# Optimization experiments

Hardware: AMD Instinct MI355X
Metric: run time of the kernel (lower is better)

## Reference

```python
import jax, jax.numpy as jnp
import numpy as np

H = 11          # hidden size
L = 5           # num layers
G = 4 * H       # gates (i,f,g,o) per PyTorch order


def run_dir(x, Wih, Whh, b, reverse):
    """Single-direction LSTM over x [B,T,D] -> [B,T,H]."""
    pre = jnp.einsum('btd,gd->btg', x, Wih) + b      # [B,T,4H] input projections
    pre = pre.transpose(1, 0, 2)                     # [T,B,4H]
    if reverse:
        pre = pre[::-1]
    B = x.shape[0]
    h0 = jnp.zeros((B, H), x.dtype)
    c0 = jnp.zeros((B, H), x.dtype)

    def step(carry, gt):
        h, c = carry
        g = gt + h @ Whh.T                           # [B,4H]
        i, f, gg, o = jnp.split(g, 4, axis=-1)
        i = jax.nn.sigmoid(i)
        f = jax.nn.sigmoid(f)
        gg = jnp.tanh(gg)
        o = jax.nn.sigmoid(o)
        c = f * c + i * gg
        h = o * jnp.tanh(c)
        return (h, c), h

    _, hs = jax.lax.scan(step, (h0, c0), pre)        # hs [T,B,H]
    if reverse:
        hs = hs[::-1]
    return hs.transpose(1, 0, 2)                     # [B,T,H]


def setup_inputs() -> dict:
    key = jax.random.key(0)
    ks = jax.random.split(key, 6)
    x = jax.random.normal(ks[0], (2048, 1, 32, 512), dtype=jnp.float32)
    # PyTorch LSTM params: layer0 input=1; layers1-4 input=2H (bidir concat)
    W_ih0 = jax.random.normal(ks[1], (2, G, 1), dtype=jnp.float32) * 0.2
    W_ih_rest = jax.random.normal(ks[2], (L - 1, 2, G, 2 * H), dtype=jnp.float32) * 0.1
    W_hh = jax.random.normal(ks[3], (L, 2, G, H), dtype=jnp.float32) * 0.1
    b_ih = jax.random.normal(ks[4], (L, 2, G), dtype=jnp.float32) * 0.05
    b_hh = jax.random.normal(ks[5], (L, 2, G), dtype=jnp.float32) * 0.05
    return {"x": x, "W_ih0": W_ih0, "W_ih_rest": W_ih_rest, "W_hh": W_hh,
            "b_ih": b_ih, "b_hh": b_hh}


def reference(x, W_ih0, W_ih_rest, W_hh, b_ih, b_hh):
    # x: [B, C=1, height, width] -> sum over height -> [B, C, W] -> [B, W, C]
    inp = x.sum(2).transpose(0, 2, 1)                # [B, W, 1]
    for l in range(L):
        outs = []
        for d in range(2):                           # 0=fwd, 1=bwd
            Wih = W_ih0[d] if l == 0 else W_ih_rest[l - 1, d]
            b = b_ih[l, d] + b_hh[l, d]
            outs.append(run_dir(inp, Wih, W_hh[l, d], b, reverse=(d == 1)))
        inp = jnp.concatenate(outs, axis=-1)         # [B, W, 2H]
    return inp
```

## Files before the change

### kernel.cpp

```cpp
#include <hip/hip_runtime.h>

constexpr int TT = 512;
constexpr int BB = 2048;
constexpr int HH = 11;
constexpr int GG = 44;
constexpr int NL = 5;

typedef float v2f __attribute__((ext_vector_type(2)));

__device__ __forceinline__ float dpp_q0(float v) {
    return __int_as_float(__builtin_amdgcn_mov_dpp(__float_as_int(v), 0x00, 0xF, 0xF, false));
}
__device__ __forceinline__ float dpp_q1(float v) {
    return __int_as_float(__builtin_amdgcn_mov_dpp(__float_as_int(v), 0x55, 0xF, 0xF, false));
}
__device__ __forceinline__ float dpp_q3(float v) {
    return __int_as_float(__builtin_amdgcn_mov_dpp(__float_as_int(v), 0xFF, 0xF, 0xF, false));
}
__device__ __forceinline__ float dpp_qswap2(float v) {
    return __int_as_float(__builtin_amdgcn_mov_dpp(__float_as_int(v), 0x4E, 0xF, 0xF, false));
}

__global__ void reduce_x(const float* __restrict__ x, float* __restrict__ inp) {
    int t = blockIdx.x * 256 + threadIdx.x;
    int b = blockIdx.y;
    const float* p = x + (size_t)b * 32 * TT + t;
    float s = 0.f;
#pragma unroll
    for (int k = 0; k < 32; k++) s += p[k * TT];
    inp[(size_t)b * TT + t] = s;
}

template <int IND>
__global__ __launch_bounds__(256, 4)
void lstm_layer(
    const float* __restrict__ xin,
    float* __restrict__ out,
    const float* __restrict__ Wih,
    const float* __restrict__ Whh,
    const float* __restrict__ bih,
    const float* __restrict__ bhh)
{
    constexpr int NP   = (IND > 1) ? IND / 2 : 1;
    constexpr int CH   = (IND == 1) ? 64 : 32;
    constexpr int NCH  = TT / CH;
    constexpr int NLD  = (CH * IND) / 64;
    constexpr int PERW = 64 + 2 * CH * IND;

    __shared__ float smem[4 * PERW];

    const float L2E   = 1.4426950408889634f;
    const float NL2E  = -L2E;
    const float N2L2E = -2.f * L2E;

    int tid  = threadIdx.x;
    int lane = tid & 63;
    int wid  = tid >> 6;
    int u = lane >> 2;
    int q = lane & 3;
    bool active = (u < HH);
    int grow = q * HH + u;

    int seq = __builtin_amdgcn_readfirstlane((int)blockIdx.x * 4 + wid);
    int b = seq >> 1;
    int d = seq & 1;

    float esc    = (q == 2) ? N2L2E : NL2E;
    float ascale = (q == 2) ? 2.f * N2L2E : 1.f;
    float aoff   = (q == 2) ? -N2L2E : 0.f;

    v2f   wih2[NP];
    float wih0 = 0.f;
    v2f   whh2[6];
    v2f   bias2;
    if (active) {
        const float* wi = Wih + (size_t)(d * GG + grow) * IND;
        if constexpr (IND == 1) {
            wih0 = wi[0] * esc;
        } else {
#pragma unroll
            for (int p = 0; p < NP; p++) wih2[p] = ((const v2f*)wi)[p] * esc;
        }
        const float* wh = Whh + (size_t)(d * GG + grow) * HH;
#pragma unroll
        for (int k = 0; k < 5; k++)
            whh2[k] = (v2f){wh[2 * k] * esc, wh[2 * k + 1] * esc};
        whh2[5] = (v2f){wh[10] * esc, 0.f};
        float bv = (bih[d * GG + grow] + bhh[d * GG + grow]) * esc;
        bias2 = (v2f){bv, 0.f};
    } else {
        if constexpr (IND != 1) {
#pragma unroll
            for (int p = 0; p < NP; p++) wih2[p] = (v2f){0.f, 0.f};
        }
#pragma unroll
        for (int k = 0; k < 6; k++) whh2[k] = (v2f){0.f, 0.f};
        bias2 = (v2f){0.f, 0.f};
    }

    v2f hp[6];
#pragma unroll
    for (int k = 0; k < 6; k++) hp[k] = (v2f){0.f, 0.f};
    float c = 0.f;

    const int ostep = d ? -22 : 22;
    float* op = out + (size_t)b * TT * 22 + (size_t)(d ? (TT - 1) * 22 : 0)
                    + d * HH + u;
    const bool doStore = (q == 0) && active;

    float* shh = smem + wid * PERW;
    float* xls = shh + 64;

    const float* gbase = xin + (size_t)b * TT * IND
                             + (size_t)(d ? (TT - CH) * IND : 0);
    const int gstep = d ? -(CH * IND) : (CH * IND);
    const int lstep = d ? -IND : IND;

    {
        float p0[NLD];
#pragma unroll
        for (int k = 0; k < NLD; k++) p0[k] = gbase[k * 64 + lane];
#pragma unroll
        for (int k = 0; k < NLD; k++) xls[k * 64 + lane] = p0[k];
    }
    int buf = 0;
    float* swc = xls;
    const float* lrow = swc + (d ? (CH - 1) * IND : 0);

    v2f   xA[NP], xB[NP];
    float xAs = 0.f, xBs = 0.f;
    if constexpr (IND == 1) {
        xAs = lrow[0];
    } else {
#pragma unroll
        for (int p = 0; p < NP; p++) xA[p] = ((const v2f*)lrow)[p];
    }

    const float* gnext = gbase + gstep;

#define LSTM_STEP(XC, XN, DOPF)                                               \
    do {                                                                      \
        v2f accA, accB;                                                       \
        float pre;                                                            \
        if constexpr (IND == 1) {                                             \
            accA = __builtin_elementwise_fma(hp[0], whh2[0], bias2);          \
            accB = hp[1] * whh2[1];                                           \
            _Pragma("unroll")                                                 \
            for (int k = 2; k < 6; k++) {                                     \
                if (k & 1) accB = __builtin_elementwise_fma(hp[k], whh2[k], accB);\
                else       accA = __builtin_elementwise_fma(hp[k], whh2[k], accA);\
            }                                                                 \
            v2f s = accA + accB;                                              \
            pre = fmaf(XC##s, wih0, s.x + s.y);                               \
            if (DOPF) { lrow += lstep; XN##s = lrow[0]; }                     \
        } else {                                                              \
               \
            accA = __builtin_elementwise_fma(XC[0], wih2[0], bias2);          \
            accB = XC[1] * wih2[1];                                           \
            _Pragma("unroll")                                                 \
            for (int p = 2; p < NP; p++) {                                    \
                if (p & 1) accB = __builtin_elementwise_fma(XC[p], wih2[p], accB);\
                else       accA = __builtin_elementwise_fma(XC[p], wih2[p], accA);\
            }                                                                 \
            if (DOPF) {              \
                lrow += lstep;                                                \
                _Pragma("unroll")                                             \
                for (int p = 0; p < NP; p++) XN[p] = ((const v2f*)lrow)[p];   \
            }                                                                 \
                                                              \
            _Pragma("unroll")                                                 \
            for (int k = 0; k < 6; k++) {                                     \
                if (k & 1) accB = __builtin_elementwise_fma(hp[k], whh2[k], accB);\
                else       accA = __builtin_elementwise_fma(hp[k], whh2[k], accA);\
            }                                                                 \
            v2f s = accA + accB;                                              \
            pre = s.x + s.y;                                                  \
        }                                                                     \
        float e   = __builtin_amdgcn_exp2f(pre);                              \
        float act = fmaf(ascale, __builtin_amdgcn_rcpf(1.f + e), aoff);       \
        float ig  = act * dpp_qswap2(act);                 \
        float igb = dpp_q0(ig);                                               \
        float fv  = dpp_q1(act);                                              \
        float ov  = dpp_q3(act);                                              \
        c = fmaf(fv, c, igb);                                                 \
        float e2 = __builtin_amdgcn_exp2f(c);                                 \
        float th = fmaf(2.f, __builtin_amdgcn_rcpf(1.f + e2), -1.f);          \
        float h  = ov * th;                                 \
        if (doStore) *op = h;                                                 \
        op += ostep;                                                          \
            \
        shh[lane] = h;                                                        \
        _Pragma("unroll")                                                     \
        for (int k = 0; k < 6; k++)                                           \
            hp[k] = (v2f){shh[8 * k], shh[8 * k + 4]};                        \
    } while (0)

    for (int ch = 0; ch < NCH; ch++) {
        const bool last = (ch + 1 == NCH);
        float pf[NLD];
        if (!last) {
#pragma unroll
            for (int k = 0; k < NLD; k++) pf[k] = gnext[k * 64 + lane];
        }
        for (int sl = 0; sl < CH - 2; sl += 2) {
            LSTM_STEP(xA, xB, true);
            LSTM_STEP(xB, xA, true);
        }
        LSTM_STEP(xA, xB, true);
        LSTM_STEP(xB, xA, false);
        if (!last) {
            float* swn = xls + ((buf ^ 1) ? CH * IND : 0);
#pragma unroll
            for (int k = 0; k < NLD; k++) swn[k * 64 + lane] = pf[k];
            buf ^= 1;
            swc = swn;
            lrow = swc + (d ? (CH - 1) * IND : 0);
            if constexpr (IND == 1) {
                xAs = lrow[0];
            } else {
#pragma unroll
                for (int p = 0; p < NP; p++) xA[p] = ((const v2f*)lrow)[p];
            }
            gnext += gstep;
        }
    }
#undef LSTM_STEP
}

extern "C" void kernel_launch(void* const* d_in, const int* in_sizes, int n_in,
                              void* d_out, int out_size, void* d_ws, size_t ws_size,
                              hipStream_t stream) {
    const float* x        = (const float*)d_in[0];
    const float* W_ih0    = (const float*)d_in[1];
    const float* W_ih_rest= (const float*)d_in[2];
    const float* W_hh     = (const float*)d_in[3];
    const float* b_ih     = (const float*)d_in[4];
    const float* b_hh     = (const float*)d_in[5];
    float* out = (float*)d_out;

    const size_t perB = (size_t)TT * 22 * sizeof(float);
    int chunk = BB;
    while (chunk > 2 && (size_t)chunk * perB > ws_size) chunk >>= 1;
    float* wsbuf = (float*)d_ws;

    for (int c0 = 0; c0 < BB; c0 += chunk) {
        const float* xc   = x + (size_t)c0 * 32 * TT;
        float*       outc = out + (size_t)c0 * TT * 22;
        const int nblk = (chunk * 2) / 4;

        reduce_x<<<dim3(2, chunk), 256, 0, stream>>>(xc, wsbuf);

        lstm_layer<1><<<nblk, 256, 0, stream>>>(wsbuf, outc, W_ih0, W_hh, b_ih, b_hh);

        for (int l = 1; l < NL; l++) {
            const float* src = (l & 1) ? outc : wsbuf;
            float*       dst = (l & 1) ? wsbuf : outc;
            lstm_layer<22><<<nblk, 256, 0, stream>>>(
                src, dst,
                W_ih_rest + (size_t)(l - 1) * 2 * GG * 22,
                W_hh + (size_t)l * 2 * GG * HH,
                b_ih + (size_t)l * 2 * GG,
                b_hh + (size_t)l * 2 * GG);
        }
    }
}
```

Baseline: 1.427 ms.

## Broadcast hidden state via readlane to SGPRs instead of LDS round trip

Replaces the per-step LDS write/read of the hidden state with inline-asm v_readlane into scalar registers feeding packed FMAs, removing an LDS store/load and its wait from the serial recurrence. It also re-lays the staged input rows into a padded, direction-normalized layout (row stride 24, reversed for backward) so each timestep's input row loads as 16-byte vectors with a constant positive stride. The cost is that readlane-to-SGPR-to-VALU dependencies can stall, and hardcoded SGPR clobbers s20-s31 constrain register allocation.

```diff
diff --git a/kernel.cpp b/kernel.cpp
--- a/kernel.cpp
+++ b/kernel.cpp
@@ -7,6 +7,7 @@
 constexpr int NL = 5;
 
 typedef float v2f __attribute__((ext_vector_type(2)));
+typedef float v4f __attribute__((ext_vector_type(4)));
 
 __device__ __forceinline__ float dpp_q0(float v) {
     return __int_as_float(__builtin_amdgcn_mov_dpp(__float_as_int(v), 0x00, 0xF, 0xF, false));
@@ -41,13 +42,14 @@
     const float* __restrict__ bih,
     const float* __restrict__ bhh)
 {
-    constexpr int NP   = (IND > 1) ? IND / 2 : 1;
-    constexpr int CH   = (IND == 1) ? 64 : 32;
-    constexpr int NCH  = TT / CH;
-    constexpr int NLD  = (CH * IND) / 64;
-    constexpr int PERW = 64 + 2 * CH * IND;
-
-    __shared__ float smem[4 * PERW];
+    constexpr int NP    = (IND > 1) ? IND / 2 : 1;
+    constexpr int CH    = (IND == 1) ? 64 : 32;
+    constexpr int NCH   = TT / CH;
+    constexpr int NLD   = (CH * IND) / 64;
+    constexpr int RS    = (IND == 1) ? 1 : 24;
+    constexpr int BUFSZ = CH * RS;
+
+    __shared__ __align__(16) float smem[4 * 2 * BUFSZ];
 
     const float L2E   = 1.4426950408889634f;
     const float NL2E  = -L2E;
@@ -98,9 +100,7 @@
         bias2 = (v2f){0.f, 0.f};
     }
 
-    v2f hp[6];
-#pragma unroll
-    for (int k = 0; k < 6; k++) hp[k] = (v2f){0.f, 0.f};
+    float hprev = 0.f;
     float c = 0.f;
 
     const int ostep = d ? -22 : 22;
@@ -108,53 +108,60 @@
                     + d * HH + u;
     const bool doStore = (q == 0) && active;
 
-    float* shh = smem + wid * PERW;
-    float* xls = shh + 64;
+    float* xls = smem + wid * (2 * BUFSZ);
 
     const float* gbase = xin + (size_t)b * TT * IND
                              + (size_t)(d ? (TT - CH) * IND : 0);
     const int gstep = d ? -(CH * IND) : (CH * IND);
-    const int lstep = d ? -IND : IND;
+
+    int wdw[NLD];
+#pragma unroll
+    for (int k = 0; k < NLD; k++) {
+        int p = k * 64 + lane;
+        int row = p / IND;
+        int col = p - row * IND;
+        int r2 = d ? (CH - 1 - row) : row;
+        wdw[k] = r2 * RS + col;
+    }
 
     {
         float p0[NLD];
 #pragma unroll
         for (int k = 0; k < NLD; k++) p0[k] = gbase[k * 64 + lane];
 #pragma unroll
-        for (int k = 0; k < NLD; k++) xls[k * 64 + lane] = p0[k];
+        for (int k = 0; k < NLD; k++) xls[wdw[k]] = p0[k];
     }
     int buf = 0;
-    float* swc = xls;
-    const float* lrow = swc + (d ? (CH - 1) * IND : 0);
+    const float* lrow = xls;
+    const float* gnext = gbase + gstep;
 
     v2f   xA[NP], xB[NP];
     float xAs = 0.f, xBs = 0.f;
-    if constexpr (IND == 1) {
-        xAs = lrow[0];
-    } else {
-#pragma unroll
-        for (int p = 0; p < NP; p++) xA[p] = ((const v2f*)lrow)[p];
-    }
-
-    const float* gnext = gbase + gstep;
+
+#define LOAD_ROW(DST, PTR)                                                    \
+    do {                                                                      \
+        if constexpr (IND == 1) {                                             \
+            DST##s = (PTR)[0];                                                \
+        } else {                                                              \
+            _Pragma("unroll")                                                 \
+            for (int i4 = 0; i4 < 5; i4++) {                                  \
+                v4f t4 = ((const v4f*)(PTR))[i4];                             \
+                DST[2 * i4]     = (v2f){t4.x, t4.y};                          \
+                DST[2 * i4 + 1] = (v2f){t4.z, t4.w};                          \
+            }                                                                 \
+            DST[10] = ((const v2f*)(PTR))[10];                                \
+        }                                                                     \
+    } while (0)
+
+    LOAD_ROW(xA, lrow);
 
 #define LSTM_STEP(XC, XN, DOPF)                                               \
     do {                                                                      \
         v2f accA, accB;                                                       \
-        float pre;                                                            \
         if constexpr (IND == 1) {                                             \
-            accA = __builtin_elementwise_fma(hp[0], whh2[0], bias2);          \
-            accB = hp[1] * whh2[1];                                           \
-            _Pragma("unroll")                                                 \
-            for (int k = 2; k < 6; k++) {                                     \
-                if (k & 1) accB = __builtin_elementwise_fma(hp[k], whh2[k], accB);\
-                else       accA = __builtin_elementwise_fma(hp[k], whh2[k], accA);\
-            }                                                                 \
-            v2f s = accA + accB;                                              \
-            pre = fmaf(XC##s, wih0, s.x + s.y);                               \
-            if (DOPF) { lrow += lstep; XN##s = lrow[0]; }                     \
+            accA = bias2;                                                     \
+            accB = (v2f){0.f, 0.f};                                           \
         } else {                                                              \
-               \
             accA = __builtin_elementwise_fma(XC[0], wih2[0], bias2);          \
             accB = XC[1] * wih2[1];                                           \
             _Pragma("unroll")                                                 \
@@ -162,23 +169,39 @@
                 if (p & 1) accB = __builtin_elementwise_fma(XC[p], wih2[p], accB);\
                 else       accA = __builtin_elementwise_fma(XC[p], wih2[p], accA);\
             }                                                                 \
-            if (DOPF) {              \
-                lrow += lstep;                                                \
-                _Pragma("unroll")                                             \
-                for (int p = 0; p < NP; p++) XN[p] = ((const v2f*)lrow)[p];   \
-            }                                                                 \
-                                                              \
-            _Pragma("unroll")                                                 \
-            for (int k = 0; k < 6; k++) {                                     \
-                if (k & 1) accB = __builtin_elementwise_fma(hp[k], whh2[k], accB);\
-                else       accA = __builtin_elementwise_fma(hp[k], whh2[k], accA);\
-            }                                                                 \
-            v2f s = accA + accB;                                              \
-            pre = s.x + s.y;                                                  \
         }                                                                     \
+        if (DOPF) { lrow += RS; LOAD_ROW(XN, lrow); }                         \
+            \
+        asm volatile(                                                         \
+            "v_readlane_b32 s20, %2, 0\n\t"                                   \
+            "v_readlane_b32 s21, %2, 4\n\t"                                   \
+            "v_readlane_b32 s22, %2, 8\n\t"                                   \
+            "v_readlane_b32 s23, %2, 12\n\t"                                  \
+            "v_readlane_b32 s24, %2, 16\n\t"                                  \
+            "v_readlane_b32 s25, %2, 20\n\t"                                  \
+            "v_readlane_b32 s26, %2, 24\n\t"                                  \
+            "v_readlane_b32 s27, %2, 28\n\t"                                  \
+            "v_readlane_b32 s28, %2, 32\n\t"                                  \
+            "v_readlane_b32 s29, %2, 36\n\t"                                  \
+            "v_readlane_b32 s30, %2, 40\n\t"                                  \
+            "v_readlane_b32 s31, %2, 44\n\t"                                  \
+            "v_pk_fma_f32 %0, s[20:21], %3, %0\n\t"                           \
+            "v_pk_fma_f32 %1, s[22:23], %4, %1\n\t"                           \
+            "v_pk_fma_f32 %0, s[24:25], %5, %0\n\t"                           \
+            "v_pk_fma_f32 %1, s[26:27], %6, %1\n\t"                           \
+            "v_pk_fma_f32 %0, s[28:29], %7, %0\n\t"                           \
+            "v_pk_fma_f32 %1, s[30:31], %8, %1"                               \
+            : "+v"(accA), "+v"(accB)                                          \
+            : "v"(hprev), "v"(whh2[0]), "v"(whh2[1]), "v"(whh2[2]),           \
+              "v"(whh2[3]), "v"(whh2[4]), "v"(whh2[5])                        \
+            : "s20","s21","s22","s23","s24","s25","s26","s27",                \
+              "s28","s29","s30","s31");                                       \
+        v2f s2 = accA + accB;                                                 \
+        float pre = s2.x + s2.y;                                              \
+        if constexpr (IND == 1) pre = fmaf(XC##s, wih0, pre);                 \
         float e   = __builtin_amdgcn_exp2f(pre);                              \
         float act = fmaf(ascale, __builtin_amdgcn_rcpf(1.f + e), aoff);       \
-        float ig  = act * dpp_qswap2(act);                 \
+        float ig  = act * dpp_qswap2(act);                  \
         float igb = dpp_q0(ig);                                               \
         float fv  = dpp_q1(act);                                              \
         float ov  = dpp_q3(act);                                              \
@@ -188,11 +211,7 @@
         float h  = ov * th;                                 \
         if (doStore) *op = h;                                                 \
         op += ostep;                                                          \
-            \
-        shh[lane] = h;                                                        \
-        _Pragma("unroll")                                                     \
-        for (int k = 0; k < 6; k++)                                           \
-            hp[k] = (v2f){shh[8 * k], shh[8 * k + 4]};                        \
+        hprev = h;                                                            \
     } while (0)
 
     for (int ch = 0; ch < NCH; ch++) {
@@ -209,22 +228,17 @@
         LSTM_STEP(xA, xB, true);
         LSTM_STEP(xB, xA, false);
         if (!last) {
-            float* swn = xls + ((buf ^ 1) ? CH * IND : 0);
-#pragma unroll
-            for (int k = 0; k < NLD; k++) swn[k * 64 + lane] = pf[k];
+            float* swn = xls + ((buf ^ 1) ? BUFSZ : 0);
+#pragma unroll
+            for (int k = 0; k < NLD; k++) swn[wdw[k]] = pf[k];
             buf ^= 1;
-            swc = swn;
-            lrow = swc + (d ? (CH - 1) * IND : 0);
-            if constexpr (IND == 1) {
-                xAs = lrow[0];
-            } else {
-#pragma unroll
-                for (int p = 0; p < NP; p++) xA[p] = ((const v2f*)lrow)[p];
-            }
+            lrow = swn;
+            LOAD_ROW(xA, lrow);
             gnext += gstep;
         }
     }
 #undef LSTM_STEP
+#undef LOAD_ROW
 }
 
 extern "C" void kernel_launch(void* const* d_in, const int* in_sizes, int n_in,
```

New measurement: 1.230 ms. -13.8%, faster.
